# Kernel optimization log

Measured on AMD Instinct MI355X. Metric: run time of the kernel, lower is better.

Reference implementation:

```python
import jax, jax.numpy as jnp
import numpy as np
import math

B, C, H, W, D = 4, 64, 16, 16, 16
TEMB = 256
GROUPS = 16
EPS = 1e-5


def group_norm(x, gamma, beta, groups=GROUPS, eps=EPS):
    # x: [B, C, H, W, D]
    b, c, h, w, d = x.shape
    xg = x.reshape(b, groups, c // groups, h, w, d)
    mu = jnp.mean(xg, axis=(2, 3, 4, 5), keepdims=True)
    var = jnp.var(xg, axis=(2, 3, 4, 5), keepdims=True)
    xn = ((xg - mu) / jnp.sqrt(var + eps)).reshape(b, c, h, w, d)
    return xn * gamma[None, :, None, None, None] + beta[None, :, None, None, None]


def swish(x):
    return x * jax.nn.sigmoid(x)


def conv3d(x, w, b=None):
    y = jax.lax.conv_general_dilated(
        x, w, window_strides=(1, 1, 1), padding='SAME',
        dimension_numbers=('NCDHW', 'OIDHW', 'NCDHW'))
    if b is not None:
        y = y + b[None, :, None, None, None]
    return y


def setup_inputs() -> dict:
    key = jax.random.key(0)
    ks = jax.random.split(key, 16)
    s = lambda fan: 1.0 / math.sqrt(fan)
    inp = {
        'x': jax.random.normal(ks[0], (B, C, H, W, D), jnp.float32),
        'time_emb': jax.random.normal(ks[1], (B, TEMB), jnp.float32),
        # block1: GroupNorm + Conv3d(C->C, 3)
        'gn1_g': jnp.ones((C,), jnp.float32),
        'gn1_b': jnp.zeros((C,), jnp.float32),
        'conv1_w': jax.random.normal(ks[2], (C, C, 3, 3, 3), jnp.float32) * s(C * 27),
        'conv1_b': jnp.zeros((C,), jnp.float32),
        # time-embedding MLP: Linear(TEMB -> C)
        'mlp_w': jax.random.normal(ks[3], (C, TEMB), jnp.float32) * s(TEMB),
        'mlp_b': jnp.zeros((C,), jnp.float32),
        # block2: GroupNorm + Conv3d(C->C, 3)
        'gn2_g': jnp.ones((C,), jnp.float32),
        'gn2_b': jnp.zeros((C,), jnp.float32),
        'conv2_w': jax.random.normal(ks[4], (C, C, 3, 3, 3), jnp.float32) * s(C * 27),
        'conv2_b': jnp.zeros((C,), jnp.float32),
        # attention: GroupNorm, qkv 1x1 conv (no bias), out 1x1 conv
        'agn_g': jnp.ones((C,), jnp.float32),
        'agn_b': jnp.zeros((C,), jnp.float32),
        'qkv_w': jax.random.normal(ks[5], (3 * C, C), jnp.float32) * s(C),
        'out_w': jax.random.normal(ks[6], (C, C), jnp.float32) * s(C),
        'out_b': jnp.zeros((C,), jnp.float32),
    }
    return inp


def reference(x, time_emb, gn1_g, gn1_b, conv1_w, conv1_b, mlp_w, mlp_b,
              gn2_g, gn2_b, conv2_w, conv2_b, agn_g, agn_b, qkv_w, out_w, out_b):
    # --- ResnetBlock ---
    h = conv3d(swish(group_norm(x, gn1_g, gn1_b)), conv1_w, conv1_b)
    t = swish(time_emb) @ mlp_w.T + mlp_b                    # [B, C]
    h = h + t[:, :, None, None, None]
    h = conv3d(swish(group_norm(h, gn2_g, gn2_b)), conv2_w, conv2_b)
    x = h + x                                                # res_conv is Identity (dim == dim_out)
    # --- SelfAttention (n_head = 1) ---
    b, c, hh, ww, dd = x.shape
    n = hh * ww * dd
    norm = group_norm(x, agn_g, agn_b)
    qkv = jnp.einsum('oc,bchwd->bohwd', qkv_w, norm).reshape(b, 3 * c, n)
    q, k, v = jnp.split(qkv, 3, axis=1)                      # [B, C, N] each
    attn = jnp.einsum('bcn,bcm->bnm', q, k) / math.sqrt(c)   # [B, N, N]
    attn = jax.nn.softmax(attn, axis=-1)
    o = jnp.einsum('bnm,bcm->bcn', attn, v).reshape(b, c, hh, ww, dd)
    o = jnp.einsum('oc,bchwd->bohwd', out_w, o) + out_b[None, :, None, None, None]
    return o + x
```

## Files before the change

### kernel.cpp

```cpp
#include <hip/hip_runtime.h>
#include <math.h>

#define B 4
#define C 64
#define G 16
#define CPG 4
#define N 4096
#define TEMB 256

using f16x8 = __attribute__((ext_vector_type(8))) _Float16;
using f16x4 = __attribute__((ext_vector_type(4))) _Float16;
using f32x4 = __attribute__((ext_vector_type(4))) float;
using f32x16 = __attribute__((ext_vector_type(16))) float;
using h2 = __attribute__((ext_vector_type(2))) __fp16;

#define QSCALE 0.18033688f
#define SHIFT2 4.328085f

__device__ __forceinline__ int swzi(int row, int ci) {
  return (((ci >> 3) ^ (row & 7)) << 3) | (ci & 7);
}

__device__ __forceinline__ void gn_fin(const float2* pstats, const float* gamma,
                                       const float* beta, int b, int c,
                                       float& sc, float& sh) {
  int g = c >> 2;
  const float2* ps = pstats + ((size_t)(b * 16 + g)) * 4;
  float2 p0 = ps[0], p1 = ps[1], p2 = ps[2], p3 = ps[3];
  const float inv = 1.f / 16384.f;
  float mean = (p0.x + p1.x + p2.x + p3.x) * inv;
  float msq = (p0.y + p1.y + p2.y + p3.y) * inv;
  float var = msq - mean * mean;
  float rstd = rsqrtf(var + 1e-5f);
  sc = gamma[c] * rstd;
  sh = beta[c] - mean * sc;
}

__device__ __forceinline__ void gn_fin2(const float2* red, const float* gamma,
                                        const float* beta, int b, int c,
                                        float& sc, float& sh) {
  float2 r = red[b * 16 + (c >> 2)];
  const float inv = 1.f / 16384.f;
  float mean = r.x * inv;
  float var = r.y * inv - mean * mean;
  float rstd = rsqrtf(var + 1e-5f);
  sc = gamma[c] * rstd;
  sh = beta[c] - mean * sc;
}

__global__ void __launch_bounds__(256) k_gnpart(const float* __restrict__ x,
                                                float2* __restrict__ pstats) {
  int bx = blockIdx.x;
  const float4* xp = (const float4*)(x + (size_t)bx * 4096);
  float s = 0.f, s2 = 0.f;
#pragma unroll
  for (int kk = 0; kk < 4; kk++) {
    float4 v = xp[threadIdx.x + kk * 256];
    s += v.x + v.y + v.z + v.w;
    s2 += v.x * v.x + v.y * v.y + v.z * v.z + v.w * v.w;
  }
#pragma unroll
  for (int off = 32; off > 0; off >>= 1) {
    s += __shfl_down(s, off);
    s2 += __shfl_down(s2, off);
  }
  __shared__ float ls[4], ls2[4];
  int lane = threadIdx.x & 63, wid = threadIdx.x >> 6;
  if (lane == 0) { ls[wid] = s; ls2[wid] = s2; }
  __syncthreads();
  if (threadIdx.x == 0) {
    float2 r;
    r.x = ls[0] + ls[1] + ls[2] + ls[3];
    r.y = ls2[0] + ls2[1] + ls2[2] + ls2[3];
    pstats[bx] = r;
  }
}

__global__ void k_gnred(const float2* __restrict__ blkstats, float2* __restrict__ red) {
  int tid = threadIdx.x;
  int pair = tid >> 2, q = tid & 3;
  int b = pair >> 4, g = pair & 15;
  float sx = 0.f, sy = 0.f;
  for (int i = 0; i < 16; i++) {
    float2 v = blkstats[(size_t)(b * 64 + q * 16 + i) * 16 + g];
    sx += v.x; sy += v.y;
  }
  sx += __shfl_xor(sx, 1); sy += __shfl_xor(sy, 1);
  sx += __shfl_xor(sx, 2); sy += __shfl_xor(sy, 2);
  if (q == 0) { float2 r; r.x = sx; r.y = sy; red[pair] = r; }
}

__global__ void __launch_bounds__(256) k_prep(const float* __restrict__ w1,
                                              const float* __restrict__ w2,
                                              const float* __restrict__ temb,
                                              const float* __restrict__ mlp_w,
                                              const float* __restrict__ mlp_b,
                                              _Float16* __restrict__ wf1,
                                              _Float16* __restrict__ wf2,
                                              float* __restrict__ tb) {
  int bx = blockIdx.x, tid = threadIdx.x;
  if (bx < 54) {
    const float* w = (bx < 27) ? w1 : w2;
    _Float16* wf = (bx < 27) ? wf1 : wf2;
    int tap = (bx < 27) ? bx : bx - 27;
    int co = tid >> 2, ci0 = (tid & 3) * 16;
    union { _Float16 hh[16]; f16x8 v[2]; } pk;
#pragma unroll
    for (int r = 0; r < 16; r++)
      pk.hh[r] = (_Float16)w[((size_t)(co * 64 + ci0 + r)) * 27 + tap];
    f16x8* dst = (f16x8*)(wf + ((size_t)tap * 64 + co) * 64 + ci0);
    dst[0] = pk.v[0]; dst[1] = pk.v[1];
  } else {
    int b = bx - 54;
    __shared__ float sw[TEMB];
    __shared__ float part[4][64];
    {
      float v = temb[b * TEMB + tid];
      sw[tid] = v / (1.f + __expf(-v));
    }
    __syncthreads();
    int co = tid & 63, seg = tid >> 6;
    float acc = 0.f;
#pragma unroll 16
    for (int k = 0; k < 64; k++) acc += sw[seg * 64 + k] * mlp_w[co * TEMB + seg * 64 + k];
    part[seg][co] = acc;
    __syncthreads();
    if (tid < 64) tb[b * C + tid] = part[0][tid] + part[1][tid] + part[2][tid] + part[3][tid] + mlp_b[tid];
  }
}

__global__ void __launch_bounds__(256) k_actT(const float* __restrict__ in,
                                              const float2* __restrict__ pstats,
                                              const float* __restrict__ gamma,
                                              const float* __restrict__ beta,
                                              _Float16* __restrict__ outT, int mode) {
  int b = blockIdx.x >> 6, nt = blockIdx.x & 63;
  int n0 = nt * 64;
  __shared__ float xl[64][68];
  int tid = threadIdx.x;
  {
    int c = tid >> 2, seg = tid & 3;
    float sc, sh;
    if (mode == 0) gn_fin(pstats, gamma, beta, b, c, sc, sh);
    else gn_fin2(pstats, gamma, beta, b, c, sc, sh);
    const float4* src = (const float4*)(in + ((size_t)(b * C + c)) * N + n0 + seg * 16);
#pragma unroll
    for (int j = 0; j < 4; j++) {
      float4 v = src[j];
      float t0 = v.x * sc + sh, t1 = v.y * sc + sh, t2 = v.z * sc + sh, t3 = v.w * sc + sh;
      xl[c][seg * 16 + j * 4 + 0] = t0 / (1.f + __expf(-t0));
      xl[c][seg * 16 + j * 4 + 1] = t1 / (1.f + __expf(-t1));
      xl[c][seg * 16 + j * 4 + 2] = t2 / (1.f + __expf(-t2));
      xl[c][seg * 16 + j * 4 + 3] = t3 / (1.f + __expf(-t3));
    }
  }
  __syncthreads();
  {
    int n = tid >> 2, cq = (tid & 3) * 16;
    union { _Float16 hh[16]; f16x8 v[2]; } pk;
#pragma unroll
    for (int r = 0; r < 16; r++) pk.hh[r] = (_Float16)xl[cq + r][n];
    f16x8* dst = (f16x8*)(outT + ((size_t)b * N + n0 + n) * 64 + cq);
    dst[0] = pk.v[0]; dst[1] = pk.v[1];
  }
}

__global__ void __launch_bounds__(256) k_conv3(const _Float16* __restrict__ actT,
                                               const _Float16* __restrict__ wf,
                                               const float* __restrict__ bias,
                                               const float* __restrict__ addvec,
                                               const float* __restrict__ residual,
                                               float* __restrict__ out,
                                               float2* __restrict__ blkstats) {
  int bx = blockIdx.x;
  int b = bx >> 6, h = (bx >> 2) & 15, nog = bx & 3;
  int tid = threadIdx.x;
  int wv = tid >> 6, lane = tid & 63, hi = lane >> 5, l31 = lane & 31;
  int cw = wv >> 1, nw = wv & 1;
  __shared__ _Float16 a3[3][96][64];
  __shared__ _Float16 wl[2][64][64];
  __shared__ float2 sg[16];
  if (tid < 16) { sg[tid].x = 0.f; sg[tid].y = 0.f; }
  int w0 = nog * 4 - 1;
  for (int idx = tid; idx < 2304; idx += 256) {
    int r = idx / 768, rem = idx % 768;
    int ns = rem >> 3, ci8 = rem & 7;
    int wp = w0 + (ns >> 4), dp = ns & 15;
    int hin = h + r - 1;
    f16x8 v = {};
    if ((unsigned)hin < 16u && (unsigned)wp < 16u)
      v = *(const f16x8*)(actT + (((size_t)(b * 16 + hin)) * 256 + wp * 16 + dp) * 64 + ci8 * 8);
    *(f16x8*)&a3[r][ns][swzi(ns, ci8 * 8)] = v;
  }
#pragma unroll
  for (int q = 0; q < 2; q++) {
    int chunk = tid + q * 256;
    int co = chunk >> 3, ci8 = chunk & 7;
    f16x8 v = *(const f16x8*)(wf + (size_t)co * 64 + ci8 * 8);
    *(f16x8*)&wl[0][co][swzi(co, ci8 * 8)] = v;
  }
  f32x16 acc = {};
  __syncthreads();
  int cur = 0;
  int co_r = cw * 32 + l31;
  int n_loc = nw * 32 + l31;
  int wrow = n_loc >> 4;
  int d = n_loc & 15;
  for (int t = 0; t < 27; t++) {
    f16x8 pw0 = {}, pw1 = {};
    if (t < 26) {
      pw0 = *(const f16x8*)(wf + ((size_t)(t + 1) * 64 + (tid >> 3)) * 64 + (tid & 7) * 8);
      pw1 = *(const f16x8*)(wf + ((size_t)(t + 1) * 64 + ((tid + 256) >> 3)) * 64 + (tid & 7) * 8);
    }
    int kw = (t / 3) % 3, kd = t % 3, kh = t / 9;
    int wpl = wrow + kw;
    int dp = d + kd - 1;
    bool ok = (unsigned)dp < 16u;
    int ns = wpl * 16 + dp;
#pragma unroll
    for (int c4 = 0; c4 < 4; c4++) {
      int ci = c4 * 16 + hi * 8;
      f16x8 af = *(const f16x8*)&wl[cur][co_r][swzi(co_r, ci)];
      f16x8 bf = {};
      if (ok) bf = *(const f16x8*)&a3[kh][ns][swzi(ns, ci)];
      acc = __builtin_amdgcn_mfma_f32_32x32x16_f16(af, bf, acc, 0, 0, 0);
    }
    if (t < 26) {
      *(f16x8*)&wl[cur ^ 1][tid >> 3][swzi(tid >> 3, (tid & 7) * 8)] = pw0;
      *(f16x8*)&wl[cur ^ 1][(tid + 256) >> 3][swzi((tid + 256) >> 3, (tid & 7) * 8)] = pw1;
      __syncthreads();
      cur ^= 1;
    }
  }
  int nq = nog * 64 + n_loc;
  float gs[4] = {0.f, 0.f, 0.f, 0.f}, gs2[4] = {0.f, 0.f, 0.f, 0.f};
#pragma unroll
  for (int r = 0; r < 16; r++) {
    int co = cw * 32 + (r & 3) + 8 * (r >> 2) + 4 * hi;
    size_t off = (((size_t)(b * 64 + co)) * 16 + h) * 256 + nq;
    float vv = acc[r] + bias[co] + (addvec ? addvec[b * 64 + co] : 0.f);
    if (residual) vv += residual[off];
    out[off] = vv;
    gs[r >> 2] += vv;
    gs2[r >> 2] += vv * vv;
  }
#pragma unroll
  for (int off2 = 1; off2 < 32; off2 <<= 1)
#pragma unroll
    for (int rq = 0; rq < 4; rq++) {
      gs[rq] += __shfl_xor(gs[rq], off2);
      gs2[rq] += __shfl_xor(gs2[rq], off2);
    }
  if (l31 == 0) {
#pragma unroll
    for (int rq = 0; rq < 4; rq++) {
      int g = cw * 8 + 2 * rq + hi;
      atomicAdd(&sg[g].x, gs[rq]);
      atomicAdd(&sg[g].y, gs2[rq]);
    }
  }
  __syncthreads();
  if (tid < 16) blkstats[(size_t)bx * 16 + tid] = sg[tid];
}

__global__ void __launch_bounds__(256) k_qkv(const float* __restrict__ x2,
                                             const float2* __restrict__ red,
                                             const float* __restrict__ gamma,
                                             const float* __restrict__ beta,
                                             const float* __restrict__ w,
                                             _Float16* __restrict__ qh, _Float16* __restrict__ kh,
                                             _Float16* __restrict__ vh) {
  int b = blockIdx.x >> 6, nt = blockIdx.x & 63;
  int n0 = nt * 64;
  __shared__ __align__(16) float xl[64][64];
  __shared__ float wl[192 * 64];
  int tid = threadIdx.x;
  for (int i = tid; i < 192 * 64; i += 256) wl[i] = w[i];
  {
    int c = tid >> 2, seg = tid & 3;
    float sc, sh;
    gn_fin2(red, gamma, beta, b, c, sc, sh);
    const float4* src = (const float4*)(x2 + ((size_t)(b * C + c)) * N + n0);
    float4* dst = (float4*)&xl[c][seg * 16];
#pragma unroll
    for (int j = 0; j < 4; j++) {
      float4 v = src[seg * 4 + j];
      v.x = v.x * sc + sh; v.y = v.y * sc + sh; v.z = v.z * sc + sh; v.w = v.w * sc + sh;
      dst[j] = v;
    }
  }
  __syncthreads();
  int nq = tid & 15, og = tid >> 4;
  float4 acc[12];
#pragma unroll
  for (int j = 0; j < 12; j++) acc[j] = make_float4(0.f, 0.f, 0.f, 0.f);
  for (int c = 0; c < 64; c++) {
    float4 xv = *(const float4*)&xl[c][nq * 4];
#pragma unroll
    for (int j = 0; j < 12; j++) {
      float wv = wl[(og * 12 + j) * 64 + c];
      acc[j].x += wv * xv.x; acc[j].y += wv * xv.y; acc[j].z += wv * xv.z; acc[j].w += wv * xv.w;
    }
  }
#pragma unroll
  for (int j = 0; j < 12; j++) {
    int o3 = og * 12 + j;
    if (o3 >= 128) {
      f16x4 pv;
      pv[0] = (_Float16)acc[j].x; pv[1] = (_Float16)acc[j].y;
      pv[2] = (_Float16)acc[j].z; pv[3] = (_Float16)acc[j].w;
      int c = o3 - 128;
      int t = (n0 >> 4) + (nq >> 2);
      *(f16x4*)(vh + ((size_t)(b * 256 + t) * 64 + c) * 16 + (nq & 3) * 4) = pv;
    }
  }
  __syncthreads();
#pragma unroll
  for (int j = 0; j < 12; j++) {
    int o3 = og * 12 + j;
    if (o3 < 64) {
      float4 v = acc[j];
      v.x *= QSCALE; v.y *= QSCALE; v.z *= QSCALE; v.w *= QSCALE;
      *(float4*)&xl[o3][nq * 4] = v;
    }
  }
  __syncthreads();
  {
    int n_ = tid >> 2, cs = (tid & 3) * 16;
    union { _Float16 hh[16]; uint4 u[2]; } pk;
#pragma unroll
    for (int r = 0; r < 16; r++) pk.hh[r] = (_Float16)xl[cs + r][n_];
    uint4* dst = (uint4*)(qh + ((size_t)b * N + n0 + n_) * 64 + cs);
    dst[0] = pk.u[0]; dst[1] = pk.u[1];
  }
  __syncthreads();
#pragma unroll
  for (int j = 0; j < 12; j++) {
    int o3 = og * 12 + j;
    if (o3 >= 64 && o3 < 128) *(float4*)&xl[o3 - 64][nq * 4] = acc[j];
  }
  __syncthreads();
  {
    int n_ = tid >> 2, cs = (tid & 3) * 16;
    union { _Float16 hh[16]; uint4 u[2]; } pk;
#pragma unroll
    for (int r = 0; r < 16; r++) pk.hh[r] = (_Float16)xl[cs + r][n_];
    uint4* dst = (uint4*)(kh + ((size_t)b * N + n0 + n_) * 64 + cs);
    dst[0] = pk.u[0]; dst[1] = pk.u[1];
  }
}

__global__ void __launch_bounds__(256) k_attn(const _Float16* __restrict__ q,
                                              const _Float16* __restrict__ k,
                                              const _Float16* __restrict__ v,
                                              _Float16* __restrict__ po,
                                              float* __restrict__ pl) {
  int bx = blockIdx.x;
  int s = bx >> 8, b = (bx >> 6) & 3, nt = bx & 63;
  int n0 = nt * 64;
  int tid = threadIdx.x;
  int wv = tid >> 6, lane = tid & 63, lg = lane >> 4, ll = lane & 15;
  __shared__ float ol[64][72];
  __shared__ float lsum[4][64];
  const _Float16* qp = q + (size_t)b * N * 64;
  f16x8 qf[4][2];
#pragma unroll
  for (int qb = 0; qb < 4; qb++)
#pragma unroll
    for (int ch = 0; ch < 2; ch++)
      qf[qb][ch] = *(const f16x8*)(qp + (size_t)(n0 + qb * 16 + ll) * 64 + ch * 32 + lg * 8);
  f32x4 oacc[4][4] = {};
  f32x4 lfrag[4] = {};
  const f16x4 ones = {(_Float16)1.f, (_Float16)1.f, (_Float16)1.f, (_Float16)1.f};
  const _Float16* kptr = k + (size_t)b * N * 64 + (size_t)(s * 512 + wv * 16 + ll) * 64 + lg * 8;
  const _Float16* vptr = v + ((size_t)(b * 256 + s * 32 + wv) * 64 + ll) * 16 + lg * 4;
  f16x8 kf0 = *(const f16x8*)(kptr);
  f16x8 kf1 = *(const f16x8*)(kptr + 32);
  f16x4 vf[4];
#pragma unroll
  for (int cb = 0; cb < 4; cb++) vf[cb] = *(const f16x4*)(vptr + cb * 256);
  for (int it = 0; it < 8; it++) {
    const _Float16* kptrn = kptr + 4096;
    const _Float16* vptrn = vptr + 4096;
    f32x4 sv[4];
    __builtin_amdgcn_s_setprio(1);
#pragma unroll
    for (int qb = 0; qb < 4; qb++) {
      f32x4 z = {-SHIFT2, -SHIFT2, -SHIFT2, -SHIFT2};
      z = __builtin_amdgcn_mfma_f32_16x16x32_f16(kf0, qf[qb][0], z, 0, 0, 0);
      sv[qb] = __builtin_amdgcn_mfma_f32_16x16x32_f16(kf1, qf[qb][1], z, 0, 0, 0);
    }
    __builtin_amdgcn_s_setprio(0);
    f16x8 nk0 = *(const f16x8*)(kptrn);
    f16x8 nk1 = *(const f16x8*)(kptrn + 32);
    f16x4 nv[4];
#pragma unroll
    for (int cb = 0; cb < 4; cb++) nv[cb] = *(const f16x4*)(vptrn + cb * 256);
    f16x4 pk[4];
#pragma unroll
    for (int qb = 0; qb < 4; qb++) {
      float e0 = __builtin_amdgcn_exp2f(sv[qb][0]);
      float e1 = __builtin_amdgcn_exp2f(sv[qb][1]);
      float e2 = __builtin_amdgcn_exp2f(sv[qb][2]);
      float e3 = __builtin_amdgcn_exp2f(sv[qb][3]);
      union { h2 h[2]; f16x4 v4; } u;
      u.h[0] = __builtin_amdgcn_cvt_pkrtz(e0, e1);
      u.h[1] = __builtin_amdgcn_cvt_pkrtz(e2, e3);
      pk[qb] = u.v4;
    }
    __builtin_amdgcn_s_setprio(1);
#pragma unroll
    for (int qb = 0; qb < 4; qb++) {
#pragma unroll
      for (int cb = 0; cb < 4; cb++)
        oacc[qb][cb] = __builtin_amdgcn_mfma_f32_16x16x16f16(vf[cb], pk[qb], oacc[qb][cb], 0, 0, 0);
      lfrag[qb] = __builtin_amdgcn_mfma_f32_16x16x16f16(ones, pk[qb], lfrag[qb], 0, 0, 0);
    }
    __builtin_amdgcn_s_setprio(0);
    kf0 = nk0; kf1 = nk1;
#pragma unroll
    for (int cb = 0; cb < 4; cb++) vf[cb] = nv[cb];
    kptr = kptrn; vptr = vptrn;
  }
  if (lane < 16) {
#pragma unroll
    for (int qb = 0; qb < 4; qb++) lsum[wv][qb * 16 + lane] = lfrag[qb][0];
  }
  for (int w = 0; w < 4; w++) {
    __syncthreads();
    if (wv == w) {
#pragma unroll
      for (int qb = 0; qb < 4; qb++)
#pragma unroll
        for (int cb = 0; cb < 4; cb++) {
          float* a = &ol[qb * 16 + ll][cb * 16 + 4 * lg];
          if (w == 0) {
            *(f32x4*)a = oacc[qb][cb];
          } else {
            f32x4 t = *(f32x4*)a;
            t += oacc[qb][cb];
            *(f32x4*)a = t;
          }
        }
    }
  }
  __syncthreads();
  {
    int n = tid >> 2, cq = (tid & 3) * 16;
    float lt = lsum[0][n] + lsum[1][n] + lsum[2][n] + lsum[3][n];
    float inv = 1.f / lt;
    union { _Float16 hh[16]; uint4 u[2]; } pk2;
#pragma unroll
    for (int j = 0; j < 16; j++) pk2.hh[j] = (_Float16)(ol[n][cq + j] * inv);
    uint4* dst = (uint4*)(po + ((size_t)(s * 4 + b) * N + n0 + n) * 64 + cq);
    dst[0] = pk2.u[0]; dst[1] = pk2.u[1];
    if (tid < 64)
      pl[(size_t)(s * 4 + b) * N + n0 + tid] =
          lsum[0][tid] + lsum[1][tid] + lsum[2][tid] + lsum[3][tid];
  }
}

__global__ void __launch_bounds__(256) k_outproj(const _Float16* __restrict__ po,
                                                 const float* __restrict__ pl,
                                                 const float* __restrict__ w,
                                                 const float* __restrict__ bias,
                                                 const float* __restrict__ x2,
                                                 float* __restrict__ out) {
  int b = blockIdx.x >> 6, nt = blockIdx.x & 63;
  int n0 = nt * 64;
  __shared__ __align__(16) float wl2[64][68];
  __shared__ __align__(16) float ol[64][68];
  __shared__ float wsc[8][64];
  int tid = threadIdx.x;
  if (tid < 64) {
    float l[8];
    float lt = 0.f;
#pragma unroll
    for (int s = 0; s < 8; s++) {
      l[s] = pl[((size_t)(s * 4 + b)) * N + n0 + tid];
      lt += l[s];
    }
    float inv = 1.f / lt;
#pragma unroll
    for (int s = 0; s < 8; s++) wsc[s][tid] = l[s] * inv;
  }
  for (int i = tid; i < 4096; i += 256) wl2[i >> 6][i & 63] = w[i];
  __syncthreads();
  for (int base = tid; base < 1024; base += 256) {
    int n = base >> 4, c0 = (base & 15) * 4;
    float a0 = 0.f, a1 = 0.f, a2 = 0.f, a3 = 0.f;
#pragma unroll
    for (int s = 0; s < 8; s++) {
      f16x4 pv = *(const f16x4*)&po[((size_t)(s * 4 + b) * N + n0 + n) * 64 + c0];
      float wsv = wsc[s][n];
      a0 += (float)pv[0] * wsv; a1 += (float)pv[1] * wsv;
      a2 += (float)pv[2] * wsv; a3 += (float)pv[3] * wsv;
    }
    ol[n][c0] = a0; ol[n][c0 + 1] = a1; ol[n][c0 + 2] = a2; ol[n][c0 + 3] = a3;
  }
  __syncthreads();
  int co = tid & 63, ng = tid >> 6;
  float acc16[16];
#pragma unroll
  for (int i = 0; i < 16; i++) acc16[i] = 0.f;
  for (int c4 = 0; c4 < 16; c4++) {
    float4 wv = *(const float4*)&wl2[co][c4 * 4];
#pragma unroll
    for (int i = 0; i < 16; i++) {
      float4 ov = *(const float4*)&ol[ng * 16 + i][c4 * 4];
      acc16[i] += wv.x * ov.x + wv.y * ov.y + wv.z * ov.z + wv.w * ov.w;
    }
  }
  float bv = bias[co];
  __syncthreads();
#pragma unroll
  for (int i = 0; i < 16; i++) ol[ng * 16 + i][co] = acc16[i] + bv;
  __syncthreads();
  for (int kk = 0; kk < 16; kk++) {
    int i = tid + kk * 256;
    int c2 = i >> 6, nl = i & 63;
    size_t idx = ((size_t)(b * C + c2)) * N + n0 + nl;
    out[idx] = ol[nl][c2] + x2[idx];
  }
}

extern "C" void kernel_launch(void* const* d_in, const int* in_sizes, int n_in,
                              void* d_out, int out_size, void* d_ws, size_t ws_size,
                              hipStream_t stream) {
  (void)in_sizes; (void)n_in; (void)out_size; (void)ws_size;
  const float* x       = (const float*)d_in[0];
  const float* temb    = (const float*)d_in[1];
  const float* gn1_g   = (const float*)d_in[2];
  const float* gn1_b   = (const float*)d_in[3];
  const float* conv1_w = (const float*)d_in[4];
  const float* conv1_b = (const float*)d_in[5];
  const float* mlp_w   = (const float*)d_in[6];
  const float* mlp_b   = (const float*)d_in[7];
  const float* gn2_g   = (const float*)d_in[8];
  const float* gn2_b   = (const float*)d_in[9];
  const float* conv2_w = (const float*)d_in[10];
  const float* conv2_b = (const float*)d_in[11];
  const float* agn_g   = (const float*)d_in[12];
  const float* agn_b   = (const float*)d_in[13];
  const float* qkv_w   = (const float*)d_in[14];
  const float* out_w   = (const float*)d_in[15];
  const float* out_b   = (const float*)d_in[16];
  float* out = (float*)d_out;
  float* ws = (float*)d_ws;
  const size_t F = 1048576;
  float* h        = ws;
  _Float16* qh    = (_Float16*)(ws + F);
  _Float16* khb   = qh + F;
  _Float16* vhb   = khb + F;
  float2* pst1 = (float2*)(vhb + F);
  float* tb    = (float*)(pst1 + 256);
  _Float16* wf1 = (_Float16*)(tb + 256);
  _Float16* wf2 = wf1 + 27 * 64 * 64;
  _Float16* actT = wf2 + 27 * 64 * 64;
  _Float16* po   = actT;
  float* pl      = (float*)(po + 8 * F);
  float2* pstb1  = (float2*)(pl + 131072);
  float2* pstb2  = pstb1 + 4096;
  float2* red2   = pstb2 + 4096;
  float2* red3   = red2 + 64;

  k_prep<<<58, 256, 0, stream>>>(conv1_w, conv2_w, temb, mlp_w, mlp_b, wf1, wf2, tb);
  k_gnpart<<<256, 256, 0, stream>>>(x, pst1);
  k_actT<<<256, 256, 0, stream>>>(x, pst1, gn1_g, gn1_b, actT, 0);
  k_conv3<<<256, 256, 0, stream>>>(actT, wf1, conv1_b, tb, nullptr, h, pstb1);
  k_gnred<<<1, 256, 0, stream>>>(pstb1, red2);
  k_actT<<<256, 256, 0, stream>>>(h, (const float2*)red2, gn2_g, gn2_b, actT, 1);
  k_conv3<<<256, 256, 0, stream>>>(actT, wf2, conv2_b, nullptr, x, h, pstb2);
  k_gnred<<<1, 256, 0, stream>>>(pstb2, red3);
  k_qkv<<<256, 256, 0, stream>>>(h, (const float2*)red3, agn_g, agn_b, qkv_w, qh, khb, vhb);
  k_attn<<<2048, 256, 0, stream>>>(qh, khb, vhb, po, pl);
  k_outproj<<<256, 256, 0, stream>>>(po, pl, out_w, out_b, h, out);
}
```

Before: 128.2 us.

## Halve attention key splits, double-buffer K/V loads, and compute row sums with VALU

```diff
diff --git a/kernel.cpp b/kernel.cpp
--- a/kernel.cpp
+++ b/kernel.cpp
@@ -370,18 +370,11 @@
     for (int ch = 0; ch < 2; ch++)
       qf[qb][ch] = *(const f16x8*)(qp + (size_t)(n0 + qb * 16 + ll) * 64 + ch * 32 + lg * 8);
   f32x4 oacc[4][4] = {};
-  f32x4 lfrag[4] = {};
-  const f16x4 ones = {(_Float16)1.f, (_Float16)1.f, (_Float16)1.f, (_Float16)1.f};
-  const _Float16* kptr = k + (size_t)b * N * 64 + (size_t)(s * 512 + wv * 16 + ll) * 64 + lg * 8;
-  const _Float16* vptr = v + ((size_t)(b * 256 + s * 32 + wv) * 64 + ll) * 16 + lg * 4;
-  f16x8 kf0 = *(const f16x8*)(kptr);
-  f16x8 kf1 = *(const f16x8*)(kptr + 32);
-  f16x4 vf[4];
-#pragma unroll
-  for (int cb = 0; cb < 4; cb++) vf[cb] = *(const f16x4*)(vptr + cb * 256);
-  for (int it = 0; it < 8; it++) {
-    const _Float16* kptrn = kptr + 4096;
-    const _Float16* vptrn = vptr + 4096;
+  float lacc[4] = {0.f, 0.f, 0.f, 0.f};
+  const _Float16* kptr = k + (size_t)b * N * 64 + (size_t)(s * 1024 + wv * 16 + ll) * 64 + lg * 8;
+  const _Float16* vptr = v + ((size_t)(b * 256 + s * 64 + wv) * 64 + ll) * 16 + lg * 4;
+
+  auto iter = [&](f16x8 kf0, f16x8 kf1, const f16x4 (&vf)[4]) {
     f32x4 sv[4];
     __builtin_amdgcn_s_setprio(1);
 #pragma unroll
@@ -391,11 +384,6 @@
       sv[qb] = __builtin_amdgcn_mfma_f32_16x16x32_f16(kf1, qf[qb][1], z, 0, 0, 0);
     }
     __builtin_amdgcn_s_setprio(0);
-    f16x8 nk0 = *(const f16x8*)(kptrn);
-    f16x8 nk1 = *(const f16x8*)(kptrn + 32);
-    f16x4 nv[4];
-#pragma unroll
-    for (int cb = 0; cb < 4; cb++) nv[cb] = *(const f16x4*)(vptrn + cb * 256);
     f16x4 pk[4];
 #pragma unroll
     for (int qb = 0; qb < 4; qb++) {
@@ -403,6 +391,7 @@
       float e1 = __builtin_amdgcn_exp2f(sv[qb][1]);
       float e2 = __builtin_amdgcn_exp2f(sv[qb][2]);
       float e3 = __builtin_amdgcn_exp2f(sv[qb][3]);
+      lacc[qb] += (e0 + e1) + (e2 + e3);
       union { h2 h[2]; f16x4 v4; } u;
       u.h[0] = __builtin_amdgcn_cvt_pkrtz(e0, e1);
       u.h[1] = __builtin_amdgcn_cvt_pkrtz(e2, e3);
@@ -410,21 +399,54 @@
     }
     __builtin_amdgcn_s_setprio(1);
 #pragma unroll
-    for (int qb = 0; qb < 4; qb++) {
+    for (int qb = 0; qb < 4; qb++)
 #pragma unroll
       for (int cb = 0; cb < 4; cb++)
         oacc[qb][cb] = __builtin_amdgcn_mfma_f32_16x16x16f16(vf[cb], pk[qb], oacc[qb][cb], 0, 0, 0);
-      lfrag[qb] = __builtin_amdgcn_mfma_f32_16x16x16f16(ones, pk[qb], lfrag[qb], 0, 0, 0);
-    }
     __builtin_amdgcn_s_setprio(0);
-    kf0 = nk0; kf1 = nk1;
-#pragma unroll
-    for (int cb = 0; cb < 4; cb++) vf[cb] = nv[cb];
-    kptr = kptrn; vptr = vptrn;
+  };
+
+  f16x8 ka0 = *(const f16x8*)(kptr);
+  f16x8 ka1 = *(const f16x8*)(kptr + 32);
+  f16x8 kb0 = *(const f16x8*)(kptr + 4096);
+  f16x8 kb1 = *(const f16x8*)(kptr + 4096 + 32);
+  f16x4 va[4], vb[4];
+#pragma unroll
+  for (int cb = 0; cb < 4; cb++) {
+    va[cb] = *(const f16x4*)(vptr + cb * 256);
+    vb[cb] = *(const f16x4*)(vptr + 4096 + cb * 256);
+  }
+  for (int ip = 0; ip < 8; ip++) {
+    const _Float16* kp2 = kptr + 8192;
+    const _Float16* vp2 = vptr + 8192;
+    f16x8 na0 = *(const f16x8*)(kp2);
+    f16x8 na1 = *(const f16x8*)(kp2 + 32);
+    f16x4 nva[4];
+#pragma unroll
+    for (int cb = 0; cb < 4; cb++) nva[cb] = *(const f16x4*)(vp2 + cb * 256);
+    iter(ka0, ka1, va);
+    ka0 = na0; ka1 = na1;
+#pragma unroll
+    for (int cb = 0; cb < 4; cb++) va[cb] = nva[cb];
+    f16x8 nb0 = *(const f16x8*)(kp2 + 4096);
+    f16x8 nb1 = *(const f16x8*)(kp2 + 4096 + 32);
+    f16x4 nvb[4];
+#pragma unroll
+    for (int cb = 0; cb < 4; cb++) nvb[cb] = *(const f16x4*)(vp2 + 4096 + cb * 256);
+    iter(kb0, kb1, vb);
+    kb0 = nb0; kb1 = nb1;
+#pragma unroll
+    for (int cb = 0; cb < 4; cb++) vb[cb] = nvb[cb];
+    kptr = kp2; vptr = vp2;
+  }
+#pragma unroll
+  for (int qb = 0; qb < 4; qb++) {
+    lacc[qb] += __shfl_xor(lacc[qb], 16);
+    lacc[qb] += __shfl_xor(lacc[qb], 32);
   }
   if (lane < 16) {
 #pragma unroll
-    for (int qb = 0; qb < 4; qb++) lsum[wv][qb * 16 + lane] = lfrag[qb][0];
+    for (int qb = 0; qb < 4; qb++) lsum[wv][qb * 16 + lane] = lacc[qb];
   }
   for (int w = 0; w < 4; w++) {
     __syncthreads();
@@ -470,19 +492,16 @@
   int n0 = nt * 64;
   __shared__ __align__(16) float wl2[64][68];
   __shared__ __align__(16) float ol[64][68];
-  __shared__ float wsc[8][64];
+  __shared__ float wsc[4][64];
   int tid = threadIdx.x;
   if (tid < 64) {
-    float l[8];
-    float lt = 0.f;
-#pragma unroll
-    for (int s = 0; s < 8; s++) {
-      l[s] = pl[((size_t)(s * 4 + b)) * N + n0 + tid];
-      lt += l[s];
-    }
-    float inv = 1.f / lt;
-#pragma unroll
-    for (int s = 0; s < 8; s++) wsc[s][tid] = l[s] * inv;
+    float l0 = pl[((size_t)(0 * 4 + b)) * N + n0 + tid];
+    float l1 = pl[((size_t)(1 * 4 + b)) * N + n0 + tid];
+    float l2 = pl[((size_t)(2 * 4 + b)) * N + n0 + tid];
+    float l3 = pl[((size_t)(3 * 4 + b)) * N + n0 + tid];
+    float inv = 1.f / (l0 + l1 + l2 + l3);
+    wsc[0][tid] = l0 * inv; wsc[1][tid] = l1 * inv;
+    wsc[2][tid] = l2 * inv; wsc[3][tid] = l3 * inv;
   }
   for (int i = tid; i < 4096; i += 256) wl2[i >> 6][i & 63] = w[i];
   __syncthreads();
@@ -490,7 +509,7 @@
     int n = base >> 4, c0 = (base & 15) * 4;
     float a0 = 0.f, a1 = 0.f, a2 = 0.f, a3 = 0.f;
 #pragma unroll
-    for (int s = 0; s < 8; s++) {
+    for (int s = 0; s < 4; s++) {
       f16x4 pv = *(const f16x4*)&po[((size_t)(s * 4 + b) * N + n0 + n) * 64 + c0];
       float wsv = wsc[s][n];
       a0 += (float)pv[0] * wsv; a1 += (float)pv[1] * wsv;
@@ -558,8 +577,8 @@
   _Float16* wf2 = wf1 + 27 * 64 * 64;
   _Float16* actT = wf2 + 27 * 64 * 64;
   _Float16* po   = actT;
-  float* pl      = (float*)(po + 8 * F);
-  float2* pstb1  = (float2*)(pl + 131072);
+  float* pl      = (float*)(po + 4 * F);
+  float2* pstb1  = (float2*)(pl + 65536);
   float2* pstb2  = pstb1 + 4096;
   float2* red2   = pstb2 + 4096;
   float2* red3   = red2 + 64;
@@ -573,6 +592,6 @@
   k_conv3<<<256, 256, 0, stream>>>(actT, wf2, conv2_b, nullptr, x, h, pstb2);
   k_gnred<<<1, 256, 0, stream>>>(pstb2, red3);
   k_qkv<<<256, 256, 0, stream>>>(h, (const float2*)red3, agn_g, agn_b, qkv_w, qh, khb, vhb);
-  k_attn<<<2048, 256, 0, stream>>>(qh, khb, vhb, po, pl);
+  k_attn<<<1024, 256, 0, stream>>>(qh, khb, vhb, po, pl);
   k_outproj<<<256, 256, 0, stream>>>(po, pl, out_w, out_b, h, out);
 }
```

New measurement: 119.9 us. -6.5%, faster.
